# Kernel tuning notes

Measured on AMD Instinct MI355X. Metric: run time of the kernel, lower is better.

Reference implementation:

```python
import jax, jax.numpy as jnp
from jax import lax
import numpy as np

B, C, H, W = 4, 256, 64, 64
O, KH, KW = 256, 3, 3
STR, PAD, DIL = 1, 1, 1
K = KH * KW
EPS = 1e-5


def setup_inputs() -> dict:
    key = jax.random.key(0)
    ks = jax.random.split(key, 8)
    fan = 1.0 / np.sqrt(C * KH * KW)
    return {
        "input_x": jax.random.normal(ks[0], (B, C, H, W), jnp.float32),
        # offset-generating conv (DeformConv2dPack style): 2*K channels of (dy, dx)
        "w_offset": jax.random.normal(ks[1], (2 * K, C, KH, KW), jnp.float32) * 0.01,
        "b_offset": jnp.zeros((2 * K,), jnp.float32),
        # deformable conv weight / bias
        "weight": jax.random.normal(ks[2], (O, C, KH, KW), jnp.float32) * fan,
        "bias": jax.random.normal(ks[3], (O,), jnp.float32) * 0.01,
        # BatchNorm2d params + running stats (inference mode)
        "gamma": jax.random.normal(ks[4], (O,), jnp.float32) * 0.1 + 1.0,
        "beta": jax.random.normal(ks[5], (O,), jnp.float32) * 0.1,
        "run_mean": jax.random.normal(ks[6], (O,), jnp.float32) * 0.1,
        "run_var": jax.random.uniform(ks[7], (O,), jnp.float32, 0.5, 1.5),
    }


def _bilinear_sample(img, y, x):
    """img: [B,C,H,W]; y,x: [B,K,Ho,Wo] float sample coords. Zero outside."""
    y0 = jnp.floor(y)
    x0 = jnp.floor(x)
    ly = y - y0
    lx = x - x0
    y0i = y0.astype(jnp.int32)
    x0i = x0.astype(jnp.int32)
    y1i = y0i + 1
    x1i = x0i + 1

    def valid(yi, xi):
        return ((yi >= 0) & (yi < H) & (xi >= 0) & (xi < W)).astype(img.dtype)

    # per-corner interpolation weights, zeroed when the corner is out of bounds
    w00 = (1 - ly) * (1 - lx) * valid(y0i, x0i)
    w01 = (1 - ly) * lx * valid(y0i, x1i)
    w10 = ly * (1 - lx) * valid(y1i, x0i)
    w11 = ly * lx * valid(y1i, x1i)

    y0c = jnp.clip(y0i, 0, H - 1)
    y1c = jnp.clip(y1i, 0, H - 1)
    x0c = jnp.clip(x0i, 0, W - 1)
    x1c = jnp.clip(x1i, 0, W - 1)

    gather = jax.vmap(lambda im, yi, xi: im[:, yi, xi])  # -> [B,C,K,Ho,Wo]
    out = gather(img, y0c, x0c) * w00[:, None]
    out = out + gather(img, y0c, x1c) * w01[:, None]
    out = out + gather(img, y1c, x0c) * w10[:, None]
    out = out + gather(img, y1c, x1c) * w11[:, None]
    return out  # [B,C,K,Ho,Wo]


def reference(input_x, w_offset, b_offset, weight, bias, gamma, beta, run_mean, run_var):
    # 1) generate offsets with a regular conv (DeformConv2dPack conv_offset)
    offset = lax.conv_general_dilated(
        input_x, w_offset, (STR, STR), [(PAD, PAD), (PAD, PAD)],
        rhs_dilation=(DIL, DIL), dimension_numbers=("NCHW", "OIHW", "NCHW"))
    offset = offset + b_offset[None, :, None, None]  # [B, 2K, Ho, Wo]
    Ho, Wo = offset.shape[2], offset.shape[3]
    off = offset.reshape(B, K, 2, Ho, Wo)
    dy, dx = off[:, :, 0], off[:, :, 1]  # [B,K,Ho,Wo]

    # 2) base sampling grid for each kernel tap
    ky, kx = jnp.meshgrid(jnp.arange(KH), jnp.arange(KW), indexing="ij")
    base_y = (jnp.arange(Ho) * STR - PAD)[None, :, None] + (ky.reshape(-1) * DIL)[:, None, None]
    base_x = (jnp.arange(Wo) * STR - PAD)[None, None, :] + (kx.reshape(-1) * DIL)[:, None, None]
    y = base_y.astype(input_x.dtype) + dy  # [B,K,Ho,Wo]
    x = base_x.astype(input_x.dtype) + dx

    # 3) bilinear-sampled im2col then dense contraction
    sampled = _bilinear_sample(input_x, y, x)  # [B,C,K,Ho,Wo]
    out = jnp.einsum("bckhw,ock->bohw", sampled, weight.reshape(O, C, K))
    out = out + bias[None, :, None, None]

    # 4) BatchNorm (inference, running stats) + ReLU
    inv = gamma / jnp.sqrt(run_var + EPS)
    out = out * inv[None, :, None, None] + (beta - run_mean * inv)[None, :, None, None]
    return jax.nn.relu(out)
```

## Files before the change

kernel.cpp:

```cpp
#include <hip/hip_runtime.h>
#include <math.h>

typedef __attribute__((ext_vector_type(8))) short b8;
typedef __attribute__((ext_vector_type(4))) float f4;
typedef float f4u __attribute__((ext_vector_type(4), aligned(4)));
typedef _Float16 h8 __attribute__((ext_vector_type(8)));
typedef _Float16 h2 __attribute__((ext_vector_type(2)));

#define XT2   0
#define OF2   2097152
#define WH2   2392064
#define WL2   2428928
#define AF2   3571712
#define BF2   3866624

#define BARRIER_RELAX() do {                                   \
    asm volatile("s_waitcnt lgkmcnt(0)" ::: "memory");         \
    __builtin_amdgcn_s_barrier();                              \
  } while (0)

__device__ inline ushort f2bf(float f) {
  uint u = __float_as_uint(f);
  return (ushort)((u + 0x7FFFu + ((u >> 16) & 1u)) >> 16);
}
__device__ inline h2 u2h2(uint u) { union { uint u; h2 h; } x; x.u = u; return x.h; }
__device__ inline uint h22u(h2 h) { union { uint u; h2 h; } x; x.h = h; return x.u; }
__device__ inline uint duph(float f) {
  union { _Float16 h; ushort u; } x; x.h = (_Float16)f;
  return ((uint)x.u << 16) | x.u;
}

__global__ __launch_bounds__(256) void prep0_k(
    const float* __restrict__ wof, const float* __restrict__ bias,
    const float* __restrict__ gamma, const float* __restrict__ beta,
    const float* __restrict__ mean, const float* __restrict__ var,
    float* __restrict__ ws) {
  const int tid = blockIdx.x * 256 + threadIdx.x;
  ((f4*)(ws + OF2))[tid] = f4{0.f, 0.f, 0.f, 0.f};
  if (tid < 256) {
    const float iv = gamma[tid] * rsqrtf(var[tid] + 1e-5f);
    ws[BF2 + tid] = bias[tid] * iv + beta[tid] - mean[tid] * iv;
  }
  if (tid < 9216) {
    const int l2  = tid & 63;
    const int mt  = (tid >> 6) & 1;
    const int i2  = tid >> 7;
    const int cg2 = i2 / 9;
    const int kk2 = i2 - cg2 * 9;
    const int oc  = (mt << 4) + (l2 & 15);
    const int cb2 = (cg2 << 5) + ((l2 >> 4) << 3);
    b8 ph, pl;
#pragma unroll
    for (int j = 0; j < 8; ++j) {
      const float v = (oc < 18) ? wof[((oc << 8) + cb2 + j) * 9 + kk2] : 0.f;
      const ushort h = f2bf(v);
      const float hf = __uint_as_float((uint)h << 16);
      ph[j] = (short)h;
      pl[j] = (short)f2bf(v - hf);
    }
    *(b8*)((short*)(ws + WH2) + tid * 8) = ph;
    *(b8*)((short*)(ws + WL2) + tid * 8) = pl;
  }
}

__global__ __launch_bounds__(256, 4) void mid_k(
    const float* __restrict__ x, const float* __restrict__ w,
    const float* __restrict__ gamma, const float* __restrict__ var,
    float* __restrict__ ws) {
  __shared__ __align__(16) ushort Xh[3][66][40];
  __shared__ __align__(16) ushort Xl[3][66][40];
  const int bid = blockIdx.x;
  const int t   = threadIdx.x;

  if (bid >= 3072) {
    const int tid = (bid - 3072) * 256 + t;
    const int l  = tid & 63;
    const int ot = (tid >> 6) & 15;
    const int f  = tid >> 10;
    const int o  = (ot << 4) + (l & 15);
    const float inv = gamma[o] * rsqrtf(var[o] + 1e-5f);
    const int s  = f & 1;
    const int g  = f >> 1;
    const int cw = g / 9;
    const int kk = g - cw * 9;
    const int cb = (cw << 6) + (s << 5) + ((l >> 4) << 3);
    h8 pk;
#pragma unroll
    for (int j = 0; j < 8; ++j)
      pk[j] = (_Float16)(w[((o << 8) + cb + j) * 9 + kk] * inv);
    *(h8*)((_Float16*)(ws + AF2) + tid * 8) = pk;
    return;
  }

  const int r = bid % 3;
  const int g = bid / 3;
  if (r != 2) {
    const int id  = ((g << 1) + r) * 256 + t;
    const int p   = id & 4095;
    const int cg8 = (id >> 12) & 31;
    const int b   = id >> 17;
    const float* xp = x + (((long)(b * 256 + cg8 * 8)) << 12) + p;
    _Float16* xt = (_Float16*)(ws + XT2);
    h8 pk;
#pragma unroll
    for (int j = 0; j < 8; ++j) pk[j] = (_Float16)xp[(long)j << 12];
    *(h8*)(xt + ((((long)(b << 12) + p)) << 8) + (cg8 << 3)) = pk;
    return;
  }

  const int q   = g >> 8;
  const int b   = (g >> 6) & 3;
  const int ho  = g & 63;
  const int l   = t & 63;
  const int wv  = t >> 6;
  const short* afh = (const short*)(ws + WH2);
  const short* afl = (const short*)(ws + WL2);

  for (int u = t; u < 240; u += 256) {
    const int row = u / 80, rem = u % 80;
    const int col = (rem >= 40) ? 65 : 0;
    const int c   = rem % 40;
    Xh[row][col][c] = 0;
    Xl[row][col][c] = 0;
  }

  f4 acc[2];
  acc[0] = f4{0.f, 0.f, 0.f, 0.f};
  acc[1] = f4{0.f, 0.f, 0.f, 0.f};

  const int cidx = t >> 3;
  const int j8   = t & 7;
  const float* xc = x + ((long)b << 20) + ((long)cidx << 12);
  const int col = (wv << 4) + (l & 15);
  const int qc  = (l >> 4) << 3;

  for (int it = 0; it < 2; ++it) {
    const int cg = (q << 1) + it;
    __syncthreads();
    const float* xg = xc + ((long)(cg << 5) << 12);
#pragma unroll
    for (int rep = 0; rep < 6; ++rep) {
      const int fi   = (rep << 3) + j8;
      const int row  = fi >> 4;
      const int colf = (fi & 15) << 2;
      const int y = ho - 1 + row;
      f4u v = {0.f, 0.f, 0.f, 0.f};
      if (y >= 0 && y <= 63) v = *(const f4u*)(xg + (y << 6) + colf);
#pragma unroll
      for (int qq = 0; qq < 4; ++qq) {
        const ushort h = f2bf(v[qq]);
        const float hf = __uint_as_float((uint)h << 16);
        Xh[row][colf + 1 + qq][cidx] = h;
        Xl[row][colf + 1 + qq][cidx] = f2bf(v[qq] - hf);
      }
    }
    __syncthreads();
#pragma unroll
    for (int kk = 0; kk < 9; ++kk) {
      const int ky = kk / 3, kx = kk - ky * 3;
      const int i  = cg * 9 + kk;
      const b8 ah0 = *(const b8*)(afh + ((((i << 1) + 0) << 6) + l) * 8);
      const b8 ah1 = *(const b8*)(afh + ((((i << 1) + 1) << 6) + l) * 8);
      const b8 al0 = *(const b8*)(afl + ((((i << 1) + 0) << 6) + l) * 8);
      const b8 al1 = *(const b8*)(afl + ((((i << 1) + 1) << 6) + l) * 8);
      const b8 bh = *(const b8*)&Xh[ky][col + kx][qc];
      const b8 bl = *(const b8*)&Xl[ky][col + kx][qc];
      acc[0] = __builtin_amdgcn_mfma_f32_16x16x32_bf16(ah0, bh, acc[0], 0, 0, 0);
      acc[0] = __builtin_amdgcn_mfma_f32_16x16x32_bf16(ah0, bl, acc[0], 0, 0, 0);
      acc[0] = __builtin_amdgcn_mfma_f32_16x16x32_bf16(al0, bh, acc[0], 0, 0, 0);
      acc[1] = __builtin_amdgcn_mfma_f32_16x16x32_bf16(ah1, bh, acc[1], 0, 0, 0);
      acc[1] = __builtin_amdgcn_mfma_f32_16x16x32_bf16(ah1, bl, acc[1], 0, 0, 0);
      acc[1] = __builtin_amdgcn_mfma_f32_16x16x32_bf16(al1, bh, acc[1], 0, 0, 0);
    }
  }

  const int wo = col;
  const int q4 = (l >> 4) << 2;
#pragma unroll
  for (int mt = 0; mt < 2; ++mt)
#pragma unroll
    for (int rr = 0; rr < 4; ++rr) {
      const int oc = (mt << 4) + q4 + rr;
      if (oc < 18)
        atomicAdd(&ws[OF2 + ((b * 18 + oc) << 12) + (ho << 6) + wo],
                  acc[mt][rr]);
    }
}

__global__ __launch_bounds__(512, 2) void deform_gemm_f16b(
    const float* __restrict__ ws, const float* __restrict__ bof,
    float* __restrict__ out) {
  __shared__ __align__(16) uint Bs[4][64][32];
  __shared__ uint4 dW[576];
  __shared__ int4  dP[576];

  const int t     = threadIdx.x;
  const int bid   = blockIdx.x;
  const int xcd   = bid & 7;
  const int batch = xcd >> 1;
  const int half  = xcd & 1;
  const int j     = bid >> 3;
  const int sp0   = (half << 11) + (j << 6);
  const int l     = t & 63;
  const int wv    = t >> 6;

  const int sn  = ((wv & 3) << 4) | (l & 15);
  const int cg8 = ((wv >> 2) << 2) | (l >> 4);
  const uint* xtu = (const uint*)(ws + XT2) + ((long)batch << 19);
  const _Float16* af = (const _Float16*)(ws + AF2);

  for (int u = t; u < 576; u += 512) {
    const int kk = u >> 6, s = u & 63;
    const int sp = sp0 + s;
    const int ho = sp >> 6, wo = sp & 63;
    const int ky = kk / 3, kx = kk - ky * 3;
    const float dy =
        ws[OF2 + ((batch * 18 + (kk << 1)) << 12) + sp] + bof[kk << 1];
    const float dx =
        ws[OF2 + ((batch * 18 + (kk << 1) + 1) << 12) + sp] + bof[(kk << 1) + 1];
    const float py = (float)(ho - 1 + ky) + dy;
    const float px = (float)(wo - 1 + kx) + dx;
    const float y0f = floorf(py), x0f = floorf(px);
    const float ly = py - y0f, lx = px - x0f;
    const int y0 = (int)y0f, x0 = (int)x0f;
    const int y1 = y0 + 1, x1 = x0 + 1;
    const float vy0 = (y0 >= 0 && y0 < 64) ? 1.f : 0.f;
    const float vy1 = (y1 >= 0 && y1 < 64) ? 1.f : 0.f;
    const float vx0 = (x0 >= 0 && x0 < 64) ? 1.f : 0.f;
    const float vx1 = (x1 >= 0 && x1 < 64) ? 1.f : 0.f;
    const int y0c = min(max(y0, 0), 63), y1c = min(max(y1, 0), 63);
    const int x0c = min(max(x0, 0), 63), x1c = min(max(x1, 0), 63);
    uint4 wv4;
    wv4.x = duph((1.f - ly) * (1.f - lx) * vy0 * vx0);
    wv4.y = duph((1.f - ly) * lx * vy0 * vx1);
    wv4.z = duph(ly * (1.f - lx) * vy1 * vx0);
    wv4.w = duph(ly * lx * vy1 * vx1);
    int4 pv;
    pv.x = (y0c << 6) + x0c;
    pv.y = (y0c << 6) + x1c;
    pv.z = (y1c << 6) + x0c;
    pv.w = (y1c << 6) + x1c;
    dW[u] = wv4;
    dP[u] = pv;
  }
  __syncthreads();

  f4 acc[2][4];
#pragma unroll
  for (int m = 0; m < 2; ++m)
#pragma unroll
    for (int nt = 0; nt < 4; ++nt) acc[m][nt] = f4{0.f, 0.f, 0.f, 0.f};

  uint4 cset0[4], cset1[4];
  uint4 w0v, w1v, wq; int4 pq;
  h8 aA[2][2], aN[2][2];
  int kkd, kkg, cwg;

#define FRDD(W_, P_, KK_) do { const int u_ = ((KK_) << 6) + sn;             \
    W_ = dW[u_]; P_ = dP[u_]; } while (0)

#define FGATH(DST_, P_) do {                                                 \
    const int co_ = (cwg << 5) + (cg8 << 2);                                 \
    DST_[0] = *(const uint4*)(xtu + ((P_).x << 7) + co_);                    \
    DST_[1] = *(const uint4*)(xtu + ((P_).y << 7) + co_);                    \
    DST_[2] = *(const uint4*)(xtu + ((P_).z << 7) + co_);                    \
    DST_[3] = *(const uint4*)(xtu + ((P_).w << 7) + co_);                    \
  } while (0)

#define FCOMB(CS_, WV_, BUF_) do {                                           \
    const h2 wc0_ = u2h2((WV_).x), wc1_ = u2h2((WV_).y);                     \
    const h2 wc2_ = u2h2((WV_).z), wc3_ = u2h2((WV_).w);                     \
    uint4 r_;                                                                \
    r_.x = h22u(u2h2(CS_[0].x) * wc0_ + u2h2(CS_[1].x) * wc1_ +              \
                u2h2(CS_[2].x) * wc2_ + u2h2(CS_[3].x) * wc3_);              \
    r_.y = h22u(u2h2(CS_[0].y) * wc0_ + u2h2(CS_[1].y) * wc1_ +              \
                u2h2(CS_[2].y) * wc2_ + u2h2(CS_[3].y) * wc3_);              \
    r_.z = h22u(u2h2(CS_[0].z) * wc0_ + u2h2(CS_[1].z) * wc1_ +              \
                u2h2(CS_[2].z) * wc2_ + u2h2(CS_[3].z) * wc3_);              \
    r_.w = h22u(u2h2(CS_[0].w) * wc0_ + u2h2(CS_[1].w) * wc1_ +              \
                u2h2(CS_[2].w) * wc2_ + u2h2(CS_[3].w) * wc3_);              \
    *(uint4*)&Bs[BUF_][sn][(cg8 ^ (sn & 7)) << 2] = r_;                      \
  } while (0)

#define FLOADA(I_, DST_) do {                                                \
    _Pragma("unroll")                                                        \
    for (int m = 0; m < 2; ++m)                                              \
      _Pragma("unroll")                                                      \
      for (int s = 0; s < 2; ++s) {                                          \
        const int f_ = ((I_) << 1) + s;                                      \
        DST_[m][s] = *(const h8*)(af +                                       \
            ((((f_ << 4) + (wv << 1) + m) << 6) + l) * 8);                   \
      }                                                                      \
  } while (0)

#define FMFMA(AC_, BUF_) do {                                                \
    h8 bB_[4][2];                                                            \
    _Pragma("unroll")                                                        \
    for (int nt = 0; nt < 4; ++nt)                                           \
      _Pragma("unroll")                                                      \
      for (int s = 0; s < 2; ++s) {                                          \
        const int snr_ = (nt << 4) + (l & 15);                               \
        const int ph_  = (((s << 2) + (l >> 4)) ^ (snr_ & 7)) << 2;          \
        bB_[nt][s] = *(const h8*)&Bs[BUF_][snr_][ph_];                       \
      }                                                                      \
    _Pragma("unroll")                                                        \
    for (int m = 0; m < 2; ++m)                                              \
      _Pragma("unroll")                                                      \
      for (int nt = 0; nt < 4; ++nt) {                                       \
        acc[m][nt] = __builtin_amdgcn_mfma_f32_16x16x32_f16(                 \
            AC_[m][0], bB_[nt][0], acc[m][nt], 0, 0, 0);                     \
        acc[m][nt] = __builtin_amdgcn_mfma_f32_16x16x32_f16(                 \
            AC_[m][1], bB_[nt][1], acc[m][nt], 0, 0, 0);                     \
      }                                                                      \
  } while (0)

#define FBODY2(J_) do {                                                      \
    const int je_ = (J_);                                                    \
    if (je_ < 33) { w0v = wq; FGATH(cset0, pq);                              \
      kkg++; if (kkg == 9) { kkg = 0; cwg++; } }                             \
    if (je_ < 32) { FRDD(wq, pq, kkd); kkd = (kkd == 8) ? 0 : kkd + 1; }     \
    __builtin_amdgcn_s_setprio(1);                                           \
    FMFMA(aA, (je_ & 3));                                                    \
    __builtin_amdgcn_s_setprio(0);                                           \
    if (je_ < 35) FLOADA(je_ + 1, aN);                                       \
    if (je_ < 34) FCOMB(cset1, w1v, ((je_ + 2) & 3));                        \
    const int jo_ = (J_) + 1;                                                \
    if (jo_ < 33) { w1v = wq; FGATH(cset1, pq);                              \
      kkg++; if (kkg == 9) { kkg = 0; cwg++; } }                             \
    if (jo_ < 32) { FRDD(wq, pq, kkd); kkd = (kkd == 8) ? 0 : kkd + 1; }     \
    __builtin_amdgcn_s_setprio(1);                                           \
    FMFMA(aN, (jo_ & 3));                                                    \
    __builtin_amdgcn_s_setprio(0);                                           \
    if (jo_ < 35) FLOADA(jo_ + 1, aA);                                       \
    if (jo_ < 34) FCOMB(cset0, w0v, ((jo_ + 2) & 3));                        \
    BARRIER_RELAX();                                                         \
  } while (0)

  {
    uint4 wA, wB; int4 pA;
    cwg = 0;
    FRDD(wA, pA, 0); FGATH(cset0, pA);
    FRDD(wB, pA, 1); FGATH(cset1, pA);
    FCOMB(cset0, wA, 0);
    FCOMB(cset1, wB, 1);
    FRDD(w1v, pA, 2); FGATH(cset1, pA);
    FRDD(wq, pq, 3);
    FLOADA(0, aA);
    kkd = 4; kkg = 3;
  }
  BARRIER_RELAX();

  for (int i = 0; i < 36; i += 2) FBODY2(i);

  const float* bfold = ws + BF2;
  const int quad = l >> 4;
#pragma unroll
  for (int m = 0; m < 2; ++m) {
    const int ob = (((wv << 1) + m) << 4) + (quad << 2);
    const f4 bf = *(const f4*)&bfold[ob];
#pragma unroll
    for (int nt = 0; nt < 4; ++nt) {
      const int sp = sp0 + (nt << 4) + (l & 15);
#pragma unroll
      for (int rr = 0; rr < 4; ++rr) {
        out[(((batch << 8) + ob + rr) << 12) + sp] =
            fmaxf(acc[m][nt][rr] + bf[rr], 0.f);
      }
    }
  }
}

extern "C" void kernel_launch(void* const* d_in, const int* in_sizes, int n_in,
                              void* d_out, int out_size, void* d_ws, size_t ws_size,
                              hipStream_t stream) {
  const float* x     = (const float*)d_in[0];
  const float* wof   = (const float*)d_in[1];
  const float* bof   = (const float*)d_in[2];
  const float* w     = (const float*)d_in[3];
  const float* bias  = (const float*)d_in[4];
  const float* gamma = (const float*)d_in[5];
  const float* beta  = (const float*)d_in[6];
  const float* mean  = (const float*)d_in[7];
  const float* var   = (const float*)d_in[8];
  float* out = (float*)d_out;
  float* ws  = (float*)d_ws;

  hipLaunchKernelGGL(prep0_k, dim3(288), dim3(256), 0, stream,
                     wof, bias, gamma, beta, mean, var, ws);
  hipLaunchKernelGGL(mid_k, dim3(3360), dim3(256), 0, stream,
                     x, w, gamma, var, ws);
  hipLaunchKernelGGL(deform_gemm_f16b, dim3(256), dim3(512), 0, stream,
                     ws, bof, out);
}
```

Before: 149.5 us.

## Double GEMM block to 1024 threads, one M-tile per wave, split gather by half

The deformable GEMM block grows from 512 to 1024 threads (16 waves). Each wave now owns a single 16-row output tile instead of two. The bilinear gather/combine work is split across two thread halves, each handling half the channel pair (uint2 instead of uint4). This raises wave-level parallelism and latency hiding per CU and halves per-thread registers. In exchange, occupancy drops to one block per CU, and each B-fragment LDS read is amortized over fewer MFMAs.

```diff
diff --git a/kernel.cpp b/kernel.cpp
--- a/kernel.cpp
+++ b/kernel.cpp
@@ -187,7 +187,7 @@
     }
 }
 
-__global__ __launch_bounds__(512, 2) void deform_gemm_f16b(
+__global__ __launch_bounds__(1024, 1) void deform_gemm_f16b(
     const float* __restrict__ ws, const float* __restrict__ bof,
     float* __restrict__ out) {
   __shared__ __align__(16) uint Bs[4][64][32];
@@ -204,12 +204,15 @@
   const int l     = t & 63;
   const int wv    = t >> 6;
 
-  const int sn  = ((wv & 3) << 4) | (l & 15);
-  const int cg8 = ((wv >> 2) << 2) | (l >> 4);
+  const int sl  = t & 511;
+  const int swv = sl >> 6;
+  const int hh  = t >> 9;
+  const int sn  = ((swv & 3) << 4) | (l & 15);
+  const int cg8 = ((swv >> 2) << 2) | (l >> 4);
   const uint* xtu = (const uint*)(ws + XT2) + ((long)batch << 19);
   const _Float16* af = (const _Float16*)(ws + AF2);
 
-  for (int u = t; u < 576; u += 512) {
+  for (int u = t; u < 576; u += 1024) {
     const int kk = u >> 6, s = u & 63;
     const int sp = sp0 + s;
     const int ho = sp >> 6, wo = sp & 63;
@@ -245,52 +248,43 @@
   }
   __syncthreads();
 
-  f4 acc[2][4];
-#pragma unroll
-  for (int m = 0; m < 2; ++m)
-#pragma unroll
-    for (int nt = 0; nt < 4; ++nt) acc[m][nt] = f4{0.f, 0.f, 0.f, 0.f};
-
-  uint4 cset0[4], cset1[4];
+  f4 acc[4];
+#pragma unroll
+  for (int nt = 0; nt < 4; ++nt) acc[nt] = f4{0.f, 0.f, 0.f, 0.f};
+
+  uint2 cset0[4], cset1[4];
   uint4 w0v, w1v, wq; int4 pq;
-  h8 aA[2][2], aN[2][2];
+  h8 aA[2], aN[2];
   int kkd, kkg, cwg;
 
 #define FRDD(W_, P_, KK_) do { const int u_ = ((KK_) << 6) + sn;             \
     W_ = dW[u_]; P_ = dP[u_]; } while (0)
 
 #define FGATH(DST_, P_) do {                                                 \
-    const int co_ = (cwg << 5) + (cg8 << 2);                                 \
-    DST_[0] = *(const uint4*)(xtu + ((P_).x << 7) + co_);                    \
-    DST_[1] = *(const uint4*)(xtu + ((P_).y << 7) + co_);                    \
-    DST_[2] = *(const uint4*)(xtu + ((P_).z << 7) + co_);                    \
-    DST_[3] = *(const uint4*)(xtu + ((P_).w << 7) + co_);                    \
+    const int co_ = (cwg << 5) + (cg8 << 2) + (hh << 1);                     \
+    DST_[0] = *(const uint2*)(xtu + ((P_).x << 7) + co_);                    \
+    DST_[1] = *(const uint2*)(xtu + ((P_).y << 7) + co_);                    \
+    DST_[2] = *(const uint2*)(xtu + ((P_).z << 7) + co_);                    \
+    DST_[3] = *(const uint2*)(xtu + ((P_).w << 7) + co_);                    \
   } while (0)
 
 #define FCOMB(CS_, WV_, BUF_) do {                                           \
     const h2 wc0_ = u2h2((WV_).x), wc1_ = u2h2((WV_).y);                     \
     const h2 wc2_ = u2h2((WV_).z), wc3_ = u2h2((WV_).w);                     \
-    uint4 r_;                                                                \
+    uint2 r_;                                                                \
     r_.x = h22u(u2h2(CS_[0].x) * wc0_ + u2h2(CS_[1].x) * wc1_ +              \
                 u2h2(CS_[2].x) * wc2_ + u2h2(CS_[3].x) * wc3_);              \
     r_.y = h22u(u2h2(CS_[0].y) * wc0_ + u2h2(CS_[1].y) * wc1_ +              \
                 u2h2(CS_[2].y) * wc2_ + u2h2(CS_[3].y) * wc3_);              \
-    r_.z = h22u(u2h2(CS_[0].z) * wc0_ + u2h2(CS_[1].z) * wc1_ +              \
-                u2h2(CS_[2].z) * wc2_ + u2h2(CS_[3].z) * wc3_);              \
-    r_.w = h22u(u2h2(CS_[0].w) * wc0_ + u2h2(CS_[1].w) * wc1_ +              \
-                u2h2(CS_[2].w) * wc2_ + u2h2(CS_[3].w) * wc3_);              \
-    *(uint4*)&Bs[BUF_][sn][(cg8 ^ (sn & 7)) << 2] = r_;                      \
+    *(uint2*)&Bs[BUF_][sn][((cg8 ^ (sn & 7)) << 2) + (hh << 1)] = r_;        \
   } while (0)
 
 #define FLOADA(I_, DST_) do {                                                \
     _Pragma("unroll")                                                        \
-    for (int m = 0; m < 2; ++m)                                              \
-      _Pragma("unroll")                                                      \
-      for (int s = 0; s < 2; ++s) {                                          \
-        const int f_ = ((I_) << 1) + s;                                      \
-        DST_[m][s] = *(const h8*)(af +                                       \
-            ((((f_ << 4) + (wv << 1) + m) << 6) + l) * 8);                   \
-      }                                                                      \
+    for (int s = 0; s < 2; ++s) {                                            \
+      const int f_ = ((I_) << 1) + s;                                        \
+      DST_[s] = *(const h8*)(af + ((((f_ << 4) + wv) << 6) + l) * 8);        \
+    }                                                                        \
   } while (0)
 
 #define FMFMA(AC_, BUF_) do {                                                \
@@ -304,14 +298,12 @@
         bB_[nt][s] = *(const h8*)&Bs[BUF_][snr_][ph_];                       \
       }                                                                      \
     _Pragma("unroll")                                                        \
-    for (int m = 0; m < 2; ++m)                                              \
-      _Pragma("unroll")                                                      \
-      for (int nt = 0; nt < 4; ++nt) {                                       \
-        acc[m][nt] = __builtin_amdgcn_mfma_f32_16x16x32_f16(                 \
-            AC_[m][0], bB_[nt][0], acc[m][nt], 0, 0, 0);                     \
-        acc[m][nt] = __builtin_amdgcn_mfma_f32_16x16x32_f16(                 \
-            AC_[m][1], bB_[nt][1], acc[m][nt], 0, 0, 0);                     \
-      }                                                                      \
+    for (int nt = 0; nt < 4; ++nt) {                                         \
+      acc[nt] = __builtin_amdgcn_mfma_f32_16x16x32_f16(                      \
+          AC_[0], bB_[nt][0], acc[nt], 0, 0, 0);                             \
+      acc[nt] = __builtin_amdgcn_mfma_f32_16x16x32_f16(                      \
+          AC_[1], bB_[nt][1], acc[nt], 0, 0, 0);                             \
+    }                                                                        \
   } while (0)
 
 #define FBODY2(J_) do {                                                      \
@@ -354,9 +346,8 @@
 
   const float* bfold = ws + BF2;
   const int quad = l >> 4;
-#pragma unroll
-  for (int m = 0; m < 2; ++m) {
-    const int ob = (((wv << 1) + m) << 4) + (quad << 2);
+  {
+    const int ob = (wv << 4) + (quad << 2);
     const f4 bf = *(const f4*)&bfold[ob];
 #pragma unroll
     for (int nt = 0; nt < 4; ++nt) {
@@ -364,7 +355,7 @@
 #pragma unroll
       for (int rr = 0; rr < 4; ++rr) {
         out[(((batch << 8) + ob + rr) << 12) + sp] =
-            fmaxf(acc[m][nt][rr] + bf[rr], 0.f);
+            fmaxf(acc[nt][rr] + bf[rr], 0.f);
       }
     }
   }
@@ -389,6 +380,6 @@
                      wof, bias, gamma, beta, mean, var, ws);
   hipLaunchKernelGGL(mid_k, dim3(3360), dim3(256), 0, stream,
                      x, w, gamma, var, ws);
-  hipLaunchKernelGGL(deform_gemm_f16b, dim3(256), dim3(512), 0, stream,
+  hipLaunchKernelGGL(deform_gemm_f16b, dim3(256), dim3(1024), 0, stream,
                      ws, bof, out);
 }
```

Result: slower. 180.1 us (+20.5%).
